# Kernel optimization log

Measured on AMD Instinct MI355X. Metric: run time of the kernel, lower is better.

The kernel has to match this reference:

```python
import jax, jax.numpy as jnp
import numpy as np


def ste_sign(x):
    # Forward: q(x) = +1 if x >= 0 else -1.
    # Backward: clipped straight-through estimator (identity on |x| <= 1).
    clipped = jnp.clip(x, -1.0, 1.0)
    binary = jnp.where(x >= 0, 1.0, -1.0).astype(x.dtype)
    return clipped + jax.lax.stop_gradient(binary - clipped)


BATCH = 16384
IN_FEATURES = 4096
UNITS = 512


def setup_inputs() -> dict:
    key = jax.random.key(0)
    kx, kw = jax.random.split(key)
    x = jax.random.normal(kx, (BATCH, IN_FEATURES), dtype=jnp.float32)
    # Latent full-precision kernel (kept in [-1,1]-ish range like a constrained BNN kernel)
    W = jax.random.normal(kw, (IN_FEATURES, UNITS), dtype=jnp.float32) * 0.5
    b = jnp.zeros((UNITS,), dtype=jnp.float32)
    return {"x": x, "W": W, "b": b}


def reference(x, W, b):
    # QuantizedDense: binarize inputs and kernel to +/-1, then standard dense matmul.
    xq = ste_sign(x)                # [B, F]
    Wq = ste_sign(W)                # [F, U]
    return jnp.dot(xq, Wq) + b      # [B, U]
```

## Files before the change

kernel.cpp:

```cpp
#include <hip/hip_runtime.h>
#include <stdint.h>


#define BATCH  16384
#define UNITS  512
#define KDIM   4096
#define KSTEP  64
#define NSTEP  (KDIM / KSTEP)
#define NPER8  (NSTEP / 8)
#define MROWS  64

typedef int v4i  __attribute__((ext_vector_type(4)));
typedef int v16i __attribute__((ext_vector_type(16)));

#define BARRIER()                                                              \
    do {                                                                       \
        asm volatile("s_waitcnt lgkmcnt(0)" ::: "memory");                     \
        __builtin_amdgcn_s_barrier();                                          \
        __builtin_amdgcn_sched_barrier(0);                                     \
    } while (0)

__global__ __launch_bounds__(256) void pack_w_kernel(const float* __restrict__ W,
                                                     uint8_t* __restrict__ Wb2) {
    int t  = blockIdx.x * 256 + threadIdx.x;
    int n  = t & 511;
    int k0 = (t >> 9) * 8;
    unsigned long long m = 0;
    #pragma unroll
    for (int j = 0; j < 8; ++j) {
        float v = W[(size_t)(k0 + j) * UNITS + n];
        m |= ((v < 0.f) ? 0xFFull : 0x01ull) << (8 * j);
    }
    int s  = k0 >> 6;
    int kk = k0 & 63;
    int ks = kk >> 5;
    int hi = (kk & 31) >> 4;
    int lane = (n & 31) + 32 * hi;
    size_t a = ((((size_t)s * 16 + (n >> 5)) * 2 + ks) * 64 + lane) * 16 + (kk & 15);
    *reinterpret_cast<unsigned long long*>(Wb2 + a) = m;
}

__device__ __forceinline__ uint32_t sgn4(float4 v) {
    uint32_t b0 = v.x < 0.f ? 0xFFu : 0x01u;
    uint32_t b1 = v.y < 0.f ? 0xFFu : 0x01u;
    uint32_t b2 = v.z < 0.f ? 0xFFu : 0x01u;
    uint32_t b3 = v.w < 0.f ? 0xFFu : 0x01u;
    return b0 | (b1 << 8) | (b2 << 16) | (b3 << 24);
}


#define STEP(PB, SIP, Q)                                                       \
    {                                                                          \
        const uint8_t* _b = bbase + (size_t)(8 * (Q) + (SIP)) * 32768;         \
        v4i b0 = *reinterpret_cast<const v4i*>(_b);               \
        v4i b1 = *reinterpret_cast<const v4i*>(_b + 1024);        \
        v4i b2 = *reinterpret_cast<const v4i*>(_b + 2048);        \
        v4i b3 = *reinterpret_cast<const v4i*>(_b + 3072);        \
        const uint8_t* _a = &Af[(PB) * 32768 + (SIP) * 4096 + l * 16];         \
        v4i a00 = *reinterpret_cast<const v4i*>(_a);              \
        v4i a01 = *reinterpret_cast<const v4i*>(_a + 1024);       \
        v4i a10 = *reinterpret_cast<const v4i*>(_a + 2048);       \
        v4i a11 = *reinterpret_cast<const v4i*>(_a + 3072);       \
        __builtin_amdgcn_s_setprio(1);                                         \
        acc00 = __builtin_amdgcn_mfma_i32_32x32x32_i8(a00, b0, acc00, 0, 0, 0);\
        acc00 = __builtin_amdgcn_mfma_i32_32x32x32_i8(a01, b1, acc00, 0, 0, 0);\
        acc01 = __builtin_amdgcn_mfma_i32_32x32x32_i8(a00, b2, acc01, 0, 0, 0);\
        acc01 = __builtin_amdgcn_mfma_i32_32x32x32_i8(a01, b3, acc01, 0, 0, 0);\
        acc10 = __builtin_amdgcn_mfma_i32_32x32x32_i8(a10, b0, acc10, 0, 0, 0);\
        acc10 = __builtin_amdgcn_mfma_i32_32x32x32_i8(a11, b1, acc10, 0, 0, 0);\
        acc11 = __builtin_amdgcn_mfma_i32_32x32x32_i8(a10, b2, acc11, 0, 0, 0);\
        acc11 = __builtin_amdgcn_mfma_i32_32x32x32_i8(a11, b3, acc11, 0, 0, 0);\
        __builtin_amdgcn_s_setprio(0);                                         \
    }

#define XLD2(XA, XB, S)                                                        \
    {                                                                          \
        const int _sc = ((S) < NSTEP) ? (S) : NSTEP - 1;                       \
        XA = *reinterpret_cast<const float4*>(xr0 + (size_t)_sc * KSTEP);      \
        XB = *reinterpret_cast<const float4*>(xr0 + (size_t)32 * KDIM          \
                                                  + (size_t)_sc * KSTEP);      \
    }

#define XCM2(PB, SIP, XA, XB)                                                  \
    {                                                                          \
        *reinterpret_cast<uint32_t*>(                                          \
            &Af[(PB) * 32768 + (SIP) * 4096 + awk]) = sgn4(XA);                \
        *reinterpret_cast<uint32_t*>(                                          \
            &Af[(PB) * 32768 + (SIP) * 4096 + 2048 + awk]) = sgn4(XB);         \
    }

#define PERIOD(Q, PB)                                                          \
    {                                                                          \
        STEP(PB, 0, Q);                                                        \
        XLD2(xB0, xB1, 8 * (Q) + 9);                                           \
        STEP(PB, 1, Q);                                                        \
        XCM2((PB) ^ 1, 0, xA0, xA1);                                           \
        XLD2(xA0, xA1, 8 * (Q) + 10);                                          \
        STEP(PB, 2, Q);                                                        \
        XCM2((PB) ^ 1, 1, xB0, xB1);                                           \
        XLD2(xB0, xB1, 8 * (Q) + 11);                                          \
        STEP(PB, 3, Q);                                                        \
        XCM2((PB) ^ 1, 2, xA0, xA1);                                           \
        XLD2(xA0, xA1, 8 * (Q) + 12);                                          \
        STEP(PB, 4, Q);                                                        \
        XCM2((PB) ^ 1, 3, xB0, xB1);                                           \
        XLD2(xB0, xB1, 8 * (Q) + 13);                                          \
        STEP(PB, 5, Q);                                                        \
        XCM2((PB) ^ 1, 4, xA0, xA1);                                           \
        XLD2(xA0, xA1, 8 * (Q) + 14);                                          \
        STEP(PB, 6, Q);                                                        \
        XCM2((PB) ^ 1, 5, xB0, xB1);                                           \
        XLD2(xB0, xB1, 8 * (Q) + 15);                                          \
        STEP(PB, 7, Q);                                                        \
        XCM2((PB) ^ 1, 6, xA0, xA1);                                           \
        XLD2(xA0, xA1, 8 * (Q) + 16);      \
        XCM2((PB) ^ 1, 7, xB0, xB1);                                           \
        BARRIER();                                                             \
    }

__global__ __launch_bounds__(512, 1) void mm_kernel(const float* __restrict__ x,
                                                    const uint8_t* __restrict__ Wb2,
                                                    const float* __restrict__ bias,
                                                    float* __restrict__ C) {
    __shared__ __attribute__((aligned(16))) uint8_t Af[2 * 32768];
    const int t   = threadIdx.x;
    const int l   = t & 63;
    const int wv  = t >> 6;
    const int lr  = l & 31;
    const int hi  = l >> 5;
    const int row0 = blockIdx.x * MROWS;

    const int trow = t >> 4;
    const int tak  = (t & 15) * 4;
    const int awk = (tak >> 5) * 1024
                  + (trow + 32 * ((tak >> 4) & 1)) * 16 + (tak & 15);
    const float* xr0 = x + (size_t)(row0 + trow) * KDIM + tak;
    const uint8_t* bbase = Wb2 + ((size_t)(wv * 2) * 2 * 64 + l) * 16;

    v16i acc00, acc01, acc10, acc11;
    #pragma unroll
    for (int e = 0; e < 16; ++e) { acc00[e] = 0; acc01[e] = 0;
                                   acc10[e] = 0; acc11[e] = 0; }

    float4 xA0, xA1, xB0, xB1;

    {
        float4 xa, xb;
        XLD2(xa, xb, 0); XCM2(0, 0, xa, xb);
        XLD2(xa, xb, 1); XCM2(0, 1, xa, xb);
        XLD2(xa, xb, 2); XCM2(0, 2, xa, xb);
        XLD2(xa, xb, 3); XCM2(0, 3, xa, xb);
        XLD2(xa, xb, 4); XCM2(0, 4, xa, xb);
        XLD2(xa, xb, 5); XCM2(0, 5, xa, xb);
        XLD2(xa, xb, 6); XCM2(0, 6, xa, xb);
        XLD2(xa, xb, 7); XCM2(0, 7, xa, xb);
        XLD2(xA0, xA1, 8);
        BARRIER();
    }

    #pragma unroll 1
    for (int q = 0; q < NPER8; q += 2) {
        PERIOD(q,     0);
        PERIOD(q + 1, 1);
    }

    {
        const int col0 = wv * 64 + lr;
        const int col1 = wv * 64 + 32 + lr;
        const float bv0 = bias[col0], bv1 = bias[col1];
        #pragma unroll
        for (int r = 0; r < 16; ++r) {
            int crow = (r & 3) + 8 * (r >> 2) + 4 * hi;
            C[(size_t)(row0 + crow) * UNITS + col0]      = (float)acc00[r] + bv0;
            C[(size_t)(row0 + crow) * UNITS + col1]      = (float)acc01[r] + bv1;
            C[(size_t)(row0 + 32 + crow) * UNITS + col0] = (float)acc10[r] + bv0;
            C[(size_t)(row0 + 32 + crow) * UNITS + col1] = (float)acc11[r] + bv1;
        }
    }
}

extern "C" void kernel_launch(void* const* d_in, const int* in_sizes, int n_in,
                              void* d_out, int out_size, void* d_ws, size_t ws_size,
                              hipStream_t stream) {
    const float* x = (const float*)d_in[0];
    const float* W = (const float*)d_in[1];
    const float* b = (const float*)d_in[2];
    float* out = (float*)d_out;

    uint8_t* Wb2 = (uint8_t*)d_ws;

    pack_w_kernel<<<(512 * 512) / 256, 256, 0, stream>>>(W, Wb2);
    mm_kernel<<<BATCH / MROWS, 512, 0, stream>>>(x, Wb2, b, out);
}
```

Baseline: 90.72 us.

## Stage packed W tiles through LDS with async global_load_lds double buffering

Per-step global v4i loads of the packed binary weights are replaced with global_load_lds direct-to-LDS copies into a two-slot buffer. Each step prefetches the next step's W slice while reading the current one from LDS, gated by an explicit vmcnt wait. This aims to hide global load latency for B behind the MFMA work. In exchange it adds 64KB of LDS, and it relies on the vmcnt(6) count lining up with the in-flight x loads. Each wave only reads the slice it loaded itself, so no extra barrier is used, but the hand-set wait count is fragile.

After: 93.49 us. 3.1% more time.

```diff
diff --git a/kernel.cpp b/kernel.cpp
--- a/kernel.cpp
+++ b/kernel.cpp
@@ -19,6 +19,12 @@
         __builtin_amdgcn_s_barrier();                                          \
         __builtin_amdgcn_sched_barrier(0);                                     \
     } while (0)
+
+__device__ __forceinline__ void glds16(const uint8_t* g, uint8_t* l) {
+    __builtin_amdgcn_global_load_lds(
+        (const __attribute__((address_space(1))) uint32_t*)g,
+        (__attribute__((address_space(3))) uint32_t*)l, 16, 0, 0);
+}
 
 __global__ __launch_bounds__(256) void pack_w_kernel(const float* __restrict__ W,
                                                      uint8_t* __restrict__ Wb2) {
@@ -51,11 +57,22 @@
 
 #define STEP(PB, SIP, Q)                                                       \
     {                                                                          \
-        const uint8_t* _b = bbase + (size_t)(8 * (Q) + (SIP)) * 32768;         \
-        v4i b0 = *reinterpret_cast<const v4i*>(_b);               \
-        v4i b1 = *reinterpret_cast<const v4i*>(_b + 1024);        \
-        v4i b2 = *reinterpret_cast<const v4i*>(_b + 2048);        \
-        v4i b3 = *reinterpret_cast<const v4i*>(_b + 3072);        \
+        const int _sn = (8 * (Q) + (SIP) + 1 < NSTEP) ? 8 * (Q) + (SIP) + 1    \
+                                                      : NSTEP - 1;             \
+        const uint8_t* _gs = Wb2 + (size_t)_sn * 32768 + wv * 4096             \
+                                 + (size_t)l * 16;                             \
+        uint8_t* _ls = &Bl[_sn & 1][wv * 4096];                                \
+        glds16(_gs,        _ls);                                               \
+        glds16(_gs + 1024, _ls + 1024);                                        \
+        glds16(_gs + 2048, _ls + 2048);                                        \
+        glds16(_gs + 3072, _ls + 3072);                                        \
+        asm volatile("s_waitcnt vmcnt(6)" ::: "memory");                       \
+        __builtin_amdgcn_sched_barrier(0);                                     \
+        const uint8_t* _bl = &Bl[(8 * (Q) + (SIP)) & 1][wv * 4096 + l * 16];   \
+        v4i b0 = *reinterpret_cast<const v4i*>(_bl);              \
+        v4i b1 = *reinterpret_cast<const v4i*>(_bl + 1024);       \
+        v4i b2 = *reinterpret_cast<const v4i*>(_bl + 2048);       \
+        v4i b3 = *reinterpret_cast<const v4i*>(_bl + 3072);       \
         const uint8_t* _a = &Af[(PB) * 32768 + (SIP) * 4096 + l * 16];         \
         v4i a00 = *reinterpret_cast<const v4i*>(_a);              \
         v4i a01 = *reinterpret_cast<const v4i*>(_a + 1024);       \
@@ -123,6 +140,7 @@
                                                     const float* __restrict__ bias,
                                                     float* __restrict__ C) {
     __shared__ __attribute__((aligned(16))) uint8_t Af[2 * 32768];
+    __shared__ __attribute__((aligned(16))) uint8_t Bl[2][32768];
     const int t   = threadIdx.x;
     const int l   = t & 63;
     const int wv  = t >> 6;
@@ -135,7 +153,6 @@
     const int awk = (tak >> 5) * 1024
                   + (trow + 32 * ((tak >> 4) & 1)) * 16 + (tak & 15);
     const float* xr0 = x + (size_t)(row0 + trow) * KDIM + tak;
-    const uint8_t* bbase = Wb2 + ((size_t)(wv * 2) * 2 * 64 + l) * 16;
 
     v16i acc00, acc01, acc10, acc11;
     #pragma unroll
@@ -145,6 +162,12 @@
     float4 xA0, xA1, xB0, xB1;
 
     {
+        const uint8_t* gs = Wb2 + wv * 4096 + (size_t)l * 16;
+        uint8_t* ls = &Bl[0][wv * 4096];
+        glds16(gs,        ls);
+        glds16(gs + 1024, ls + 1024);
+        glds16(gs + 2048, ls + 2048);
+        glds16(gs + 3072, ls + 3072);
         float4 xa, xb;
         XLD2(xa, xb, 0); XCM2(0, 0, xa, xb);
         XLD2(xa, xb, 1); XCM2(0, 1, xa, xb);
```

## Split K across two wave groups per block with LDS reduction

Applied to the files above, without the earlier changes.

Doubles the block to 1024 threads and splits the K dimension in half: each group of 8 waves handles 32 K-steps with its own double-buffered LDS region. After the main loop, group 1 writes its accumulators to LDS and group 0 adds them and stores the output. This is meant to add more waves per CU to hide x-load latency, since the previous launch_bounds(512,1) allowed only 8 waves. The cost is 128KB of LDS, an extra reduction pass, and twice as many threads all loading x.

Measured after the change: 314.5 us. 247% more time.

```diff
diff --git a/kernel.cpp b/kernel.cpp
--- a/kernel.cpp
+++ b/kernel.cpp
@@ -6,8 +6,7 @@
 #define UNITS  512
 #define KDIM   4096
 #define KSTEP  64
-#define NSTEP  (KDIM / KSTEP)
-#define NPER8  (NSTEP / 8)
+#define NSTEP  64
 #define MROWS  64
 
 typedef int v4i  __attribute__((ext_vector_type(4)));
@@ -51,12 +50,12 @@
 
 #define STEP(PB, SIP, Q)                                                       \
     {                                                                          \
-        const uint8_t* _b = bbase + (size_t)(8 * (Q) + (SIP)) * 32768;         \
+        const uint8_t* _b = bbase + (size_t)(sbase + 8 * (Q) + (SIP)) * 32768; \
         v4i b0 = *reinterpret_cast<const v4i*>(_b);               \
         v4i b1 = *reinterpret_cast<const v4i*>(_b + 1024);        \
         v4i b2 = *reinterpret_cast<const v4i*>(_b + 2048);        \
         v4i b3 = *reinterpret_cast<const v4i*>(_b + 3072);        \
-        const uint8_t* _a = &Af[(PB) * 32768 + (SIP) * 4096 + l * 16];         \
+        const uint8_t* _a = &Af[afbase + (PB) * 32768 + (SIP) * 4096 + l * 16];\
         v4i a00 = *reinterpret_cast<const v4i*>(_a);              \
         v4i a01 = *reinterpret_cast<const v4i*>(_a + 1024);       \
         v4i a10 = *reinterpret_cast<const v4i*>(_a + 2048);       \
@@ -73,9 +72,9 @@
         __builtin_amdgcn_s_setprio(0);                                         \
     }
 
-#define XLD2(XA, XB, S)                                                        \
-    {                                                                          \
-        const int _sc = ((S) < NSTEP) ? (S) : NSTEP - 1;                       \
+#define XLD2(XA, XB, SL)                                                       \
+    {                                                                          \
+        const int _sc = sbase + (((SL) < 32) ? (SL) : 31);                     \
         XA = *reinterpret_cast<const float4*>(xr0 + (size_t)_sc * KSTEP);      \
         XB = *reinterpret_cast<const float4*>(xr0 + (size_t)32 * KDIM          \
                                                   + (size_t)_sc * KSTEP);      \
@@ -84,9 +83,9 @@
 #define XCM2(PB, SIP, XA, XB)                                                  \
     {                                                                          \
         *reinterpret_cast<uint32_t*>(                                          \
-            &Af[(PB) * 32768 + (SIP) * 4096 + awk]) = sgn4(XA);                \
+            &Af[afbase + (PB) * 32768 + (SIP) * 4096 + awk]) = sgn4(XA);       \
         *reinterpret_cast<uint32_t*>(                                          \
-            &Af[(PB) * 32768 + (SIP) * 4096 + 2048 + awk]) = sgn4(XB);         \
+            &Af[afbase + (PB) * 32768 + (SIP) * 4096 + 2048 + awk]) = sgn4(XB);\
     }
 
 #define PERIOD(Q, PB)                                                          \
@@ -113,29 +112,34 @@
         XLD2(xB0, xB1, 8 * (Q) + 15);                                          \
         STEP(PB, 7, Q);                                                        \
         XCM2((PB) ^ 1, 6, xA0, xA1);                                           \
-        XLD2(xA0, xA1, 8 * (Q) + 16);      \
+        XLD2(xA0, xA1, 8 * (Q) + 16);                                          \
         XCM2((PB) ^ 1, 7, xB0, xB1);                                           \
         BARRIER();                                                             \
     }
 
-__global__ __launch_bounds__(512, 1) void mm_kernel(const float* __restrict__ x,
-                                                    const uint8_t* __restrict__ Wb2,
-                                                    const float* __restrict__ bias,
-                                                    float* __restrict__ C) {
-    __shared__ __attribute__((aligned(16))) uint8_t Af[2 * 32768];
+__global__ __launch_bounds__(1024, 1) void mm_kernel(const float* __restrict__ x,
+                                                     const uint8_t* __restrict__ Wb2,
+                                                     const float* __restrict__ bias,
+                                                     float* __restrict__ C) {
+    __shared__ __attribute__((aligned(16))) uint8_t Af[131072];
     const int t   = threadIdx.x;
     const int l   = t & 63;
     const int wv  = t >> 6;
+    const int grp = wv >> 3;
+    const int wvg = wv & 7;
     const int lr  = l & 31;
     const int hi  = l >> 5;
-    const int row0 = blockIdx.x * MROWS;
-
-    const int trow = t >> 4;
-    const int tak  = (t & 15) * 4;
+    const int row0  = blockIdx.x * MROWS;
+    const int sbase = grp * 32;
+    const int afbase = grp * 65536;
+
+    const int tg   = t & 511;
+    const int trow = tg >> 4;
+    const int tak  = (tg & 15) * 4;
     const int awk = (tak >> 5) * 1024
                   + (trow + 32 * ((tak >> 4) & 1)) * 16 + (tak & 15);
     const float* xr0 = x + (size_t)(row0 + trow) * KDIM + tak;
-    const uint8_t* bbase = Wb2 + ((size_t)(wv * 2) * 2 * 64 + l) * 16;
+    const uint8_t* bbase = Wb2 + ((size_t)(wvg * 2) * 2 * 64 + l) * 16;
 
     v16i acc00, acc01, acc10, acc11;
     #pragma unroll
@@ -158,23 +162,39 @@
         BARRIER();
     }
 
-    #pragma unroll 1
-    for (int q = 0; q < NPER8; q += 2) {
-        PERIOD(q,     0);
-        PERIOD(q + 1, 1);
-    }
-
-    {
-        const int col0 = wv * 64 + lr;
-        const int col1 = wv * 64 + 32 + lr;
+    PERIOD(0, 0);
+    PERIOD(1, 1);
+    PERIOD(2, 0);
+    PERIOD(3, 1);
+
+    __syncthreads();
+    int* red = reinterpret_cast<int*>(Af);
+    const int rbase = wvg * 4096 + l;
+    if (grp == 1) {
+        #pragma unroll
+        for (int r = 0; r < 16; ++r) {
+            red[rbase + (r)      * 64] = acc00[r];
+            red[rbase + (16 + r) * 64] = acc01[r];
+            red[rbase + (32 + r) * 64] = acc10[r];
+            red[rbase + (48 + r) * 64] = acc11[r];
+        }
+    }
+    __syncthreads();
+    if (grp == 0) {
+        const int col0 = wvg * 64 + lr;
+        const int col1 = wvg * 64 + 32 + lr;
         const float bv0 = bias[col0], bv1 = bias[col1];
         #pragma unroll
         for (int r = 0; r < 16; ++r) {
             int crow = (r & 3) + 8 * (r >> 2) + 4 * hi;
-            C[(size_t)(row0 + crow) * UNITS + col0]      = (float)acc00[r] + bv0;
-            C[(size_t)(row0 + crow) * UNITS + col1]      = (float)acc01[r] + bv1;
-            C[(size_t)(row0 + 32 + crow) * UNITS + col0] = (float)acc10[r] + bv0;
-            C[(size_t)(row0 + 32 + crow) * UNITS + col1] = (float)acc11[r] + bv1;
+            int s00 = acc00[r] + red[rbase + (r)      * 64];
+            int s01 = acc01[r] + red[rbase + (16 + r) * 64];
+            int s10 = acc10[r] + red[rbase + (32 + r) * 64];
+            int s11 = acc11[r] + red[rbase + (48 + r) * 64];
+            C[(size_t)(row0 + crow) * UNITS + col0]      = (float)s00 + bv0;
+            C[(size_t)(row0 + crow) * UNITS + col1]      = (float)s01 + bv1;
+            C[(size_t)(row0 + 32 + crow) * UNITS + col0] = (float)s10 + bv0;
+            C[(size_t)(row0 + 32 + crow) * UNITS + col1] = (float)s11 + bv1;
         }
     }
 }
@@ -190,5 +210,5 @@
     uint8_t* Wb2 = (uint8_t*)d_ws;
 
     pack_w_kernel<<<(512 * 512) / 256, 256, 0, stream>>>(W, Wb2);
-    mm_kernel<<<BATCH / MROWS, 512, 0, stream>>>(x, Wb2, b, out);
-}
+    mm_kernel<<<BATCH / MROWS, 1024, 0, stream>>>(x, Wb2, b, out);
+}
```
